# Kernel optimization log

Measured on AMD Instinct MI355X. Metric: run time of the kernel, lower is better.

The kernel has to match this reference:

```python
import jax, jax.numpy as jnp
import numpy as np

KL, KN, C, INIT_KL = 18, 128, 4, 12
PAD = (KL - INIT_KL) // 2 + 1  # = 4, matches int((kernel_length-initKernelLen)/2)+1
B, L = 256, 2000
K2 = KN // 2


def setup_inputs() -> dict:
    key = jax.random.key(0)
    k1, k2, k3 = jax.random.split(key, 3)
    x = jax.random.normal(k1, (B, L, C), jnp.float32)          # channel_last input [B,L,C]
    Wf = jax.random.normal(k2, (KL, C, C, K2), jnp.float32) * 0.1  # Kernel_Full_4DTensor
    Wr = jax.random.normal(k3, (KL, C, C, K2), jnp.float32) * 0.1  # Kernel_Full_4DTensorR
    # initMask(): row0 = (KL-initKL)/2, row1 = (KL+initKL)/2
    kwf = jnp.stack([jnp.full((1, K2), (KL - INIT_KL) / 2.0, jnp.float32),
                     jnp.full((1, K2), (KL + INIT_KL) / 2.0, jnp.float32)])  # [2,1,K2]
    kwr = kwf
    return {"x": x, "Wf": Wf, "Wr": Wr, "kwf": kwf, "kwr": kwr}


def _mask(kw):
    # GeneRateMask: sigmoid soft window over kernel positions, broadcast over (c1,c2)
    j = jnp.arange(KL, dtype=jnp.float32)[:, None]                       # [KL,1]
    m = jax.nn.sigmoid(j - kw[0]) + jax.nn.sigmoid(kw[1] - j) - 1.0      # [KL,K2]
    return m[:, None, None, :]                                           # [KL,1,1,K2]


def _markonv(xp, W):
    # Markov transition conv: out[b,k,i] = sum_j sum_{c,d} xp[b,c,i+j]*xp[b,d,i+j+1]*W[j,c,d,k]
    # xp: [B,C,Lp], W: [KL,C,C,K2] -> out: [B,K2,Lp-KL]
    Lout = xp.shape[2] - KL
    out = jnp.zeros((xp.shape[0], W.shape[3], Lout), xp.dtype)
    for j in range(KL):  # fixed small unrolled loop over kernel taps
        a = jax.lax.dynamic_slice_in_dim(xp, j, Lout, axis=2)       # [B,C,Lout]
        b = jax.lax.dynamic_slice_in_dim(xp, j + 1, Lout, axis=2)   # [B,C,Lout]
        out = out + jnp.einsum('bcl,bdl,cdk->bkl', a, b, W[j], optimize=True)
    return out


def reference(x, Wf, Wr, kwf, kwr):
    xc = jnp.transpose(x, (0, 2, 1))  # channel_last=1 -> [B,C,L]
    pad = ((0, 0), (0, 0), (PAD, PAD))
    xp = jnp.pad(xc, pad)
    probf = _markonv(xp, Wf * _mask(kwf))
    xr = jnp.pad(xc[:, :, ::-1], pad)  # torch.flip on length dim, then pad
    probr = _markonv(xr, Wr * _mask(kwr))
    return jnp.concatenate([probf, probr], axis=1)  # [B, KN, Lout]
```

## Files before the change

### kernel.cpp

```cpp
#include <hip/hip_runtime.h>

#define B_    256
#define L_    2000
#define KL_   18
#define K2_   64
#define KN_   128
#define PAD_  4
#define LOUT_ 1990

#define TI_   256
#define NPOS_ 274
#define PSTR_ 24

typedef __attribute__((ext_vector_type(8)))  short bf16x8;
typedef __attribute__((ext_vector_type(16))) float f32x16;

__device__ __forceinline__ unsigned short f2bf(float f) {
    unsigned u = __float_as_uint(f);
    unsigned r = (u + 0x7fffu + ((u >> 16) & 1u)) >> 16;
    return (unsigned short)r;
}
__device__ __forceinline__ float bf2f(unsigned short s) {
    return __uint_as_float(((unsigned)s) << 16);
}

__device__ __forceinline__ float4 load_x4(const float* __restrict__ x, int b, int dir, int q) {
    int m = q - PAD_;
    if (m < 0 || m >= L_) return make_float4(0.f, 0.f, 0.f, 0.f);
    int l = dir ? (L_ - 1 - m) : m;
    const float* p = x + ((size_t)b * L_ + l) * 4;
    return *reinterpret_cast<const float4*>(p);
}

__global__ __launch_bounds__(256, 2)
void markonv_mfma(const float* __restrict__ x,
                  const float* __restrict__ Wf,
                  const float* __restrict__ Wr,
                  const float* __restrict__ kwf,
                  const float* __restrict__ kwr,
                  float* __restrict__ out) {
    __shared__ __align__(16) unsigned short phi[NPOS_ * PSTR_];
    __shared__ __align__(16) unsigned short plo[NPOS_ * PSTR_];

    const int tid   = threadIdx.x;
    const int itile = blockIdx.x;
    const int b     = blockIdx.y;
    const int dir   = blockIdx.z;
    const int i0    = itile * TI_;

    const float* W  = dir ? Wr  : Wf;
    const float* kw = dir ? kwr : kwf;

    const int wave   = tid >> 6;
    const int lane   = tid & 63;
    const int kgroup = wave & 1;
    const int col    = lane & 31;
    const int cd0    = (lane >> 5) * 8;
    const int kglob  = kgroup * 32 + col;

    float kw0 = kw[kglob];
    float kw1 = kw[K2_ + kglob];
    bf16x8 af[KL_];
    #pragma unroll
    for (int j = 0; j < KL_; ++j) {
        float fj = (float)j;
        float m = 1.f / (1.f + __expf(-(fj - kw0)))
                + 1.f / (1.f + __expf(-(kw1 - fj))) - 1.f;
        #pragma unroll
        for (int e = 0; e < 8; ++e) {
            float wv = W[(size_t)(j * 16 + cd0 + e) * K2_ + kglob] * m;
            af[j][e] = (short)f2bf(wv);
        }
    }

    for (int li = tid; li < NPOS_; li += 256) {
        int q = i0 + li;
        float4 xa = load_x4(x, b, dir, q);
        float4 xb = load_x4(x, b, dir, q + 1);
        float va[4] = {xa.x, xa.y, xa.z, xa.w};
        float vb[4] = {xb.x, xb.y, xb.z, xb.w};
        unsigned short hi[16], lo[16];
        #pragma unroll
        for (int c = 0; c < 4; ++c)
            #pragma unroll
            for (int d = 0; d < 4; ++d) {
                float p = va[c] * vb[d];
                unsigned short h = f2bf(p);
                hi[c * 4 + d] = h;
                lo[c * 4 + d] = f2bf(p - bf2f(h));
            }
        unsigned* ph = (unsigned*)&phi[li * PSTR_];
        unsigned* pl = (unsigned*)&plo[li * PSTR_];
        #pragma unroll
        for (int t = 0; t < 8; ++t) {
            ph[t] = (unsigned)hi[2 * t] | ((unsigned)hi[2 * t + 1] << 16);
            pl[t] = (unsigned)lo[2 * t] | ((unsigned)lo[2 * t + 1] << 16);
        }
    }
    __syncthreads();

    const int sp0 = (wave >> 1) * 2;
    for (int spp = sp0; spp < 8; spp += 4) {
        const int s0 = spp, s1 = spp + 1;
        f32x16 a0, a1;
        #pragma unroll
        for (int r = 0; r < 16; ++r) { a0[r] = 0.f; a1[r] = 0.f; }

        const int r0 = (s0 * 32 + col) * PSTR_ + cd0;
        const int r1 = (s1 * 32 + col) * PSTR_ + cd0;
        #pragma unroll
        for (int j = 0; j < KL_; ++j) {
            bf16x8 b0h = *(const bf16x8*)&phi[r0 + j * PSTR_];
            bf16x8 b1h = *(const bf16x8*)&phi[r1 + j * PSTR_];
            bf16x8 b0l = *(const bf16x8*)&plo[r0 + j * PSTR_];
            bf16x8 b1l = *(const bf16x8*)&plo[r1 + j * PSTR_];
            a0 = __builtin_amdgcn_mfma_f32_32x32x16_bf16(af[j], b0h, a0, 0, 0, 0);
            a1 = __builtin_amdgcn_mfma_f32_32x32x16_bf16(af[j], b1h, a1, 0, 0, 0);
            a0 = __builtin_amdgcn_mfma_f32_32x32x16_bf16(af[j], b0l, a0, 0, 0, 0);
            a1 = __builtin_amdgcn_mfma_f32_32x32x16_bf16(af[j], b1l, a1, 0, 0, 0);
        }

        float* ob = out + ((size_t)b * KN_ + (size_t)dir * K2_ + kgroup * 32) * LOUT_;
        const int rbase = 4 * (lane >> 5);
        int ig0 = i0 + s0 * 32 + col;
        if (ig0 < LOUT_) {
            #pragma unroll
            for (int r = 0; r < 16; ++r) {
                int row = (r & 3) + 8 * (r >> 2) + rbase;
                ob[(size_t)row * LOUT_ + ig0] = a0[r];
            }
        }
        int ig1 = i0 + s1 * 32 + col;
        if (ig1 < LOUT_) {
            #pragma unroll
            for (int r = 0; r < 16; ++r) {
                int row = (r & 3) + 8 * (r >> 2) + rbase;
                ob[(size_t)row * LOUT_ + ig1] = a1[r];
            }
        }
    }
}

extern "C" void kernel_launch(void* const* d_in, const int* in_sizes, int n_in,
                              void* d_out, int out_size, void* d_ws, size_t ws_size,
                              hipStream_t stream) {
    const float* x   = (const float*)d_in[0];
    const float* Wf  = (const float*)d_in[1];
    const float* Wr  = (const float*)d_in[2];
    const float* kwf = (const float*)d_in[3];
    const float* kwr = (const float*)d_in[4];
    float* out = (float*)d_out;

    dim3 grid(8 , B_, 2 );
    markonv_mfma<<<grid, 256, 0, stream>>>(x, Wf, Wr, kwf, kwr, out);
}
```

Measured before the change: 321.6 us.

## Loop each block over eight batches and reuse weight fragments across them

Each block now processes 8 batch elements in sequence, so the masked weight fragments are built once and reused across them instead of being rebuilt per batch. Every wave now holds fragments for both k-groups and covers two 32-position slices for all 64 outputs, which halves the shared-memory B loads per MFMA. The LDS row stride drops from 24 to 16 shorts. The trade-off is twice the A-fragment registers, a grid of 8x32x2 blocks with less parallelism, and possible LDS bank conflicts from the 16-short stride.

```diff
diff --git a/kernel.cpp b/kernel.cpp
--- a/kernel.cpp
+++ b/kernel.cpp
@@ -10,15 +10,15 @@
 
 #define TI_   256
 #define NPOS_ 274
-#define PSTR_ 24
+#define PSTR_ 16
+#define BB_   8
 
 typedef __attribute__((ext_vector_type(8)))  short bf16x8;
 typedef __attribute__((ext_vector_type(16))) float f32x16;
 
 __device__ __forceinline__ unsigned short f2bf(float f) {
     unsigned u = __float_as_uint(f);
-    unsigned r = (u + 0x7fffu + ((u >> 16) & 1u)) >> 16;
-    return (unsigned short)r;
+    return (unsigned short)((u + 0x7fffu + ((u >> 16) & 1u)) >> 16);
 }
 __device__ __forceinline__ float bf2f(unsigned short s) {
     return __uint_as_float(((unsigned)s) << 16);
@@ -33,109 +33,106 @@
 }
 
 __global__ __launch_bounds__(256, 2)
-void markonv_mfma(const float* __restrict__ x,
-                  const float* __restrict__ Wf,
-                  const float* __restrict__ Wr,
-                  const float* __restrict__ kwf,
-                  const float* __restrict__ kwr,
-                  float* __restrict__ out) {
+void markonv_mfma2(const float* __restrict__ x,
+                   const float* __restrict__ Wf,
+                   const float* __restrict__ Wr,
+                   const float* __restrict__ kwf,
+                   const float* __restrict__ kwr,
+                   float* __restrict__ out) {
     __shared__ __align__(16) unsigned short phi[NPOS_ * PSTR_];
     __shared__ __align__(16) unsigned short plo[NPOS_ * PSTR_];
 
-    const int tid   = threadIdx.x;
-    const int itile = blockIdx.x;
-    const int b     = blockIdx.y;
-    const int dir   = blockIdx.z;
-    const int i0    = itile * TI_;
+    const int tid    = threadIdx.x;
+    const int itile  = blockIdx.x;
+    const int bgroup = blockIdx.y;
+    const int dir    = blockIdx.z;
+    const int i0     = itile * TI_;
 
     const float* W  = dir ? Wr  : Wf;
     const float* kw = dir ? kwr : kwf;
 
-    const int wave   = tid >> 6;
-    const int lane   = tid & 63;
-    const int kgroup = wave & 1;
-    const int col    = lane & 31;
-    const int cd0    = (lane >> 5) * 8;
-    const int kglob  = kgroup * 32 + col;
+    const int wave = tid >> 6;
+    const int lane = tid & 63;
+    const int col  = lane & 31;
+    const int h    = lane >> 5;
+    const int cd0  = h * 8;
 
-    float kw0 = kw[kglob];
-    float kw1 = kw[K2_ + kglob];
-    bf16x8 af[KL_];
+    bf16x8 af0[KL_], af1[KL_];
     #pragma unroll
-    for (int j = 0; j < KL_; ++j) {
-        float fj = (float)j;
-        float m = 1.f / (1.f + __expf(-(fj - kw0)))
-                + 1.f / (1.f + __expf(-(kw1 - fj))) - 1.f;
+    for (int kg = 0; kg < 2; ++kg) {
+        int kglob = kg * 32 + col;
+        float kw0 = kw[kglob];
+        float kw1 = kw[K2_ + kglob];
         #pragma unroll
-        for (int e = 0; e < 8; ++e) {
-            float wv = W[(size_t)(j * 16 + cd0 + e) * K2_ + kglob] * m;
-            af[j][e] = (short)f2bf(wv);
+        for (int j = 0; j < KL_; ++j) {
+            float fj = (float)j;
+            float m = 1.f / (1.f + __expf(-(fj - kw0)))
+                    + 1.f / (1.f + __expf(-(kw1 - fj))) - 1.f;
+            bf16x8 a;
+            #pragma unroll
+            for (int e = 0; e < 8; ++e) {
+                float wv = W[(size_t)(j * 16 + cd0 + e) * K2_ + kglob] * m;
+                a[e] = (short)f2bf(wv);
+            }
+            if (kg == 0) af0[j] = a; else af1[j] = a;
         }
     }
 
-    for (int li = tid; li < NPOS_; li += 256) {
-        int q = i0 + li;
-        float4 xa = load_x4(x, b, dir, q);
-        float4 xb = load_x4(x, b, dir, q + 1);
-        float va[4] = {xa.x, xa.y, xa.z, xa.w};
-        float vb[4] = {xb.x, xb.y, xb.z, xb.w};
-        unsigned short hi[16], lo[16];
-        #pragma unroll
-        for (int c = 0; c < 4; ++c)
+    for (int bb = 0; bb < BB_; ++bb) {
+        const int b = bgroup * BB_ + bb;
+        __syncthreads();
+
+        for (int li = tid; li < NPOS_; li += 256) {
+            int q = i0 + li;
+            float4 xa = load_x4(x, b, dir, q);
+            float4 xb = load_x4(x, b, dir, q + 1);
+            float va[4] = {xa.x, xa.y, xa.z, xa.w};
+            float vb[4] = {xb.x, xb.y, xb.z, xb.w};
+            unsigned* ph = (unsigned*)&phi[li * PSTR_];
+            unsigned* pl = (unsigned*)&plo[li * PSTR_];
             #pragma unroll
-            for (int d = 0; d < 4; ++d) {
-                float p = va[c] * vb[d];
-                unsigned short h = f2bf(p);
-                hi[c * 4 + d] = h;
-                lo[c * 4 + d] = f2bf(p - bf2f(h));
-            }
-        unsigned* ph = (unsigned*)&phi[li * PSTR_];
-        unsigned* pl = (unsigned*)&plo[li * PSTR_];
-        #pragma unroll
-        for (int t = 0; t < 8; ++t) {
-            ph[t] = (unsigned)hi[2 * t] | ((unsigned)hi[2 * t + 1] << 16);
-            pl[t] = (unsigned)lo[2 * t] | ((unsigned)lo[2 * t + 1] << 16);
-        }
-    }
-    __syncthreads();
-
-    const int sp0 = (wave >> 1) * 2;
-    for (int spp = sp0; spp < 8; spp += 4) {
-        const int s0 = spp, s1 = spp + 1;
-        f32x16 a0, a1;
-        #pragma unroll
-        for (int r = 0; r < 16; ++r) { a0[r] = 0.f; a1[r] = 0.f; }
-
-        const int r0 = (s0 * 32 + col) * PSTR_ + cd0;
-        const int r1 = (s1 * 32 + col) * PSTR_ + cd0;
-        #pragma unroll
-        for (int j = 0; j < KL_; ++j) {
-            bf16x8 b0h = *(const bf16x8*)&phi[r0 + j * PSTR_];
-            bf16x8 b1h = *(const bf16x8*)&phi[r1 + j * PSTR_];
-            bf16x8 b0l = *(const bf16x8*)&plo[r0 + j * PSTR_];
-            bf16x8 b1l = *(const bf16x8*)&plo[r1 + j * PSTR_];
-            a0 = __builtin_amdgcn_mfma_f32_32x32x16_bf16(af[j], b0h, a0, 0, 0, 0);
-            a1 = __builtin_amdgcn_mfma_f32_32x32x16_bf16(af[j], b1h, a1, 0, 0, 0);
-            a0 = __builtin_amdgcn_mfma_f32_32x32x16_bf16(af[j], b0l, a0, 0, 0, 0);
-            a1 = __builtin_amdgcn_mfma_f32_32x32x16_bf16(af[j], b1l, a1, 0, 0, 0);
-        }
-
-        float* ob = out + ((size_t)b * KN_ + (size_t)dir * K2_ + kgroup * 32) * LOUT_;
-        const int rbase = 4 * (lane >> 5);
-        int ig0 = i0 + s0 * 32 + col;
-        if (ig0 < LOUT_) {
-            #pragma unroll
-            for (int r = 0; r < 16; ++r) {
-                int row = (r & 3) + 8 * (r >> 2) + rbase;
-                ob[(size_t)row * LOUT_ + ig0] = a0[r];
+            for (int c = 0; c < 4; ++c) {
+                #pragma unroll
+                for (int d = 0; d < 4; d += 2) {
+                    float p0 = va[c] * vb[d];
+                    float p1 = va[c] * vb[d + 1];
+                    unsigned short h0 = f2bf(p0), h1 = f2bf(p1);
+                    unsigned short l0 = f2bf(p0 - bf2f(h0)), l1 = f2bf(p1 - bf2f(h1));
+                    ph[c * 2 + d / 2] = (unsigned)h0 | ((unsigned)h1 << 16);
+                    pl[c * 2 + d / 2] = (unsigned)l0 | ((unsigned)l1 << 16);
+                }
             }
         }
-        int ig1 = i0 + s1 * 32 + col;
-        if (ig1 < LOUT_) {
+        __syncthreads();
+
+        #pragma unroll
+        for (int ss = 0; ss < 2; ++ss) {
+            const int s = wave * 2 + ss;
+            f32x16 c0, c1;
             #pragma unroll
-            for (int r = 0; r < 16; ++r) {
-                int row = (r & 3) + 8 * (r >> 2) + rbase;
-                ob[(size_t)row * LOUT_ + ig1] = a1[r];
+            for (int r = 0; r < 16; ++r) { c0[r] = 0.f; c1[r] = 0.f; }
+
+            const int base = (s * 32 + col) * PSTR_ + cd0;
+            #pragma unroll
+            for (int j = 0; j < KL_; ++j) {
+                bf16x8 bh = *(const bf16x8*)&phi[base + j * PSTR_];
+                bf16x8 bl = *(const bf16x8*)&plo[base + j * PSTR_];
+                c0 = __builtin_amdgcn_mfma_f32_32x32x16_bf16(af0[j], bh, c0, 0, 0, 0);
+                c1 = __builtin_amdgcn_mfma_f32_32x32x16_bf16(af1[j], bh, c1, 0, 0, 0);
+                c0 = __builtin_amdgcn_mfma_f32_32x32x16_bf16(af0[j], bl, c0, 0, 0, 0);
+                c1 = __builtin_amdgcn_mfma_f32_32x32x16_bf16(af1[j], bl, c1, 0, 0, 0);
+            }
+
+            const int ig = i0 + s * 32 + col;
+            if (ig < LOUT_) {
+                float* ob = out + ((size_t)b * KN_ + (size_t)dir * K2_) * LOUT_ + ig;
+                const int rbase = 4 * h;
+                #pragma unroll
+                for (int r = 0; r < 16; ++r) {
+                    int row = (r & 3) + 8 * (r >> 2) + rbase;
+                    ob[(size_t)row * LOUT_] = c0[r];
+                    ob[(size_t)(row + 32) * LOUT_] = c1[r];
+                }
             }
         }
     }
@@ -151,6 +148,6 @@
     const float* kwr = (const float*)d_in[4];
     float* out = (float*)d_out;
 
-    dim3 grid(8 , B_, 2 );
-    markonv_mfma<<<grid, 256, 0, stream>>>(x, Wf, Wr, kwf, kwr, out);
+    dim3 grid(8 , B_ / BB_, 2 );
+    markonv_mfma2<<<grid, 256, 0, stream>>>(x, Wf, Wr, kwf, kwr, out);
 }
```

New measurement: 375.3 us. 16.7% more time.
